# Kernel tuning notes

Hardware: AMD Instinct MI355X
Metric: run time of the kernel (lower is better)

## Reference

```python
import jax, jax.numpy as jnp
import numpy as np

N = 6144
IN_F = 128
OUT_F = 128
H = 4
OUT_PER_HEAD = OUT_F // H  # 32
ALPHA = 0.2  # leaky relu slope
NEG_BIG = -9e15


def setup_inputs() -> dict:
    key = jax.random.key(0)
    k1, k2, k3, k4 = jax.random.split(key, 4)
    h_mat = jax.random.normal(k1, (N, IN_F), dtype=jnp.float32)
    adj = (jax.random.uniform(k2, (N, N)) < 0.05).astype(jnp.float32)
    # glorot-ish scaled params
    weight = jax.random.normal(k3, (IN_F, H * OUT_PER_HEAD), dtype=jnp.float32) * (1.0 / np.sqrt(IN_F))
    att_weight = jax.random.normal(k4, (H, 2 * OUT_PER_HEAD), dtype=jnp.float32) * (1.0 / np.sqrt(OUT_PER_HEAD))
    return {"h_mat": h_mat, "adj": adj, "weight": weight, "att_weight": att_weight}


def reference(h_mat, adj, weight, att_weight):
    n = h_mat.shape[0]
    # W h : [n, H, f]
    wh = jnp.matmul(h_mat, weight).reshape(n, H, OUT_PER_HEAD)
    a_src = att_weight[:, :OUT_PER_HEAD]   # [H, f]
    a_dst = att_weight[:, OUT_PER_HEAD:]   # [H, f]
    logit_parent = jnp.einsum("nhf,hf->nh", wh, a_src)  # [n, H]
    logit_child = jnp.einsum("nhf,hf->nh", wh, a_dst)   # [n, H]
    # e_{ij,h} = leaky_relu(parent_i + child_j) : [n, n, H]
    e = jax.nn.leaky_relu(logit_parent[:, None, :] + logit_child[None, :, :], ALPHA)
    att = jnp.where(adj[..., None] > 0, e, NEG_BIG)
    att = jax.nn.softmax(att, axis=1)  # softmax over source nodes j
    # dropout is identity in inference mode (enable_dropout=False)
    h_prime = jnp.einsum("njh,jhf->nhf", att, wh)
    return h_prime.reshape(n, -1)  # concat=True -> [n, out_features]
```

## Files before the change

kernel.cpp:

```cpp
#include <hip/hip_runtime.h>
#include <hip/hip_bf16.h>
#include <stdint.h>
#include <stddef.h>

#define GN 6144
#define GH 4
#define HALF 3072
#define MAXD2 256

typedef float  f32x2  __attribute__((ext_vector_type(2)));
typedef float  f32x4  __attribute__((ext_vector_type(4)));
typedef float  f32x16 __attribute__((ext_vector_type(16)));
typedef __bf16 bf16x8 __attribute__((ext_vector_type(8)));

__device__ __forceinline__ float fast_exp2(float x) {
#if __has_builtin(__builtin_amdgcn_exp2f)
  return __builtin_amdgcn_exp2f(x);
#else
  return exp2f(x);
#endif
}

__global__ __launch_bounds__(256) void gat_wh(const float* __restrict__ hm,
                                              const float* __restrict__ wgt,
                                              const float* __restrict__ aw,
                                              __bf16* __restrict__ whR,
                                              float* __restrict__ lp2,
                                              float* __restrict__ lc2) {
  __shared__ float ldsC[64 * 132];
  const int t = threadIdx.x;
  const int wave = t >> 6, lane = t & 63;
  const int col = lane & 31, kg = lane >> 5;
  const int n0 = blockIdx.x * 64;
  const int rowHalf = (wave & 1) * 32;
  const int colBase = (wave >> 1) * 64;

  f32x16 acc[2];
#pragma unroll
  for (int ct = 0; ct < 2; ++ct)
#pragma unroll
    for (int i = 0; i < 16; ++i) acc[ct][i] = 0.0f;

#pragma unroll
  for (int kk = 0; kk < 8; ++kk) {
    const int k = kk * 16 + kg * 8;
    const f32x4 h0 = *(const f32x4*)(hm + (size_t)(n0 + rowHalf + col) * 128 + k);
    const f32x4 h1 = *(const f32x4*)(hm + (size_t)(n0 + rowHalf + col) * 128 + k + 4);
    bf16x8 af;
#pragma unroll
    for (int e = 0; e < 4; ++e) { af[e] = (__bf16)h0[e]; af[e + 4] = (__bf16)h1[e]; }
#pragma unroll
    for (int ct = 0; ct < 2; ++ct) {
      bf16x8 bfr;
#pragma unroll
      for (int e = 0; e < 8; ++e)
        bfr[e] = (__bf16)wgt[(size_t)(k + e) * 128 + colBase + ct * 32 + col];
      acc[ct] = __builtin_amdgcn_mfma_f32_32x32x16_bf16(af, bfr, acc[ct], 0, 0, 0);
    }
  }
#pragma unroll
  for (int ct = 0; ct < 2; ++ct)
#pragma unroll
    for (int r = 0; r < 16; ++r)
      ldsC[(rowHalf + (r & 3) + 8 * (r >> 2) + 4 * kg) * 132 + colBase + ct * 32 + col] =
          acc[ct][r];
  __syncthreads();

  {
    const int rr = t >> 2, cg = (t & 3) * 32;
    __bf16* dst = whR + (size_t)(n0 + rr) * 128 + cg;
#pragma unroll
    for (int q = 0; q < 4; ++q) {
      bf16x8 v;
#pragma unroll
      for (int e = 0; e < 8; ++e) v[e] = (__bf16)ldsC[rr * 132 + cg + q * 8 + e];
      *(bf16x8*)(dst + q * 8) = v;
    }
  }
  {
    const int nl = t & 63, h = t >> 6;
    float sp = 0.f, sd = 0.f;
#pragma unroll
    for (int f = 0; f < 32; ++f) {
      const float v = ldsC[nl * 132 + h * 32 + f];
      sp = fmaf(v, aw[h * 64 + f], sp);
      sd = fmaf(v, aw[h * 64 + 32 + f], sd);
    }
    const float LOG2E = 1.4426950408889634f;
    lp2[(n0 + nl) * GH + h] = sp * LOG2E;
    lc2[(n0 + nl) * GH + h] = sd * LOG2E;
  }
}

__global__ __launch_bounds__(256) void gat_fused(const float* __restrict__ adj,
                                                 const __bf16* __restrict__ whR,
                                                 const float* __restrict__ lp2,
                                                 const float* __restrict__ lc2,
                                                 float* __restrict__ out) {
  __shared__ unsigned short jidx[4][MAXD2];
  __shared__ float els[4][256];
  __shared__ float accx[4][64][2];
  __shared__ float denx[4][4];
  const int t = threadIdx.x, wave = t >> 6, lane = t & 63;
  const int row = blockIdx.x * 2 + (wave >> 1);
  const int half = wave & 1;
  const float* arow = adj + (size_t)row * GN + half * HALF;

  unsigned base = 0;
  f32x4 a0 = *(const f32x4*)(arow + lane * 4);
  f32x4 a1 = *(const f32x4*)(arow + 256 + lane * 4);
  for (int c = 0; c < 12; ++c) {
    f32x4 a2;
    if (c + 2 < 12) a2 = *(const f32x4*)(arow + (c + 2) * 256 + lane * 4);
#pragma unroll
    for (int s = 0; s < 4; ++s) {
      const bool p = a0[s] > 0.f;
      const unsigned long long m = __ballot(p);
      const unsigned rank = (unsigned)__popcll(m & ((1ull << lane) - 1ull));
      const unsigned pos = base + rank;
      if (p && pos < MAXD2)
        jidx[wave][pos] = (unsigned short)(half * HALF + c * 256 + lane * 4 + s);
      base += (unsigned)__popcll(m);
    }
    a0 = a1; a1 = a2;
  }
  int dg = (int)base;
  if (dg > MAXD2) dg = MAXD2;
  for (int k = dg + lane; k < MAXD2; k += 64) jidx[wave][k] = 0;

  const f32x4 lpv = *(const f32x4*)(lp2 + (size_t)row * GH);
  const int hsel = lane >> 4;
  float acc0 = 0.f, acc1 = 0.f;
  f32x2 d01 = f32x2{0.f, 0.f}, d23 = f32x2{0.f, 0.f};

  const int nch = (dg + 63) >> 6;
  for (int c = 0; c < nch; ++c) {
    const int k = c * 64 + lane;
    const bool valid = k < dg;
    const int jv = valid ? (int)jidx[wave][k] : 0;
    const f32x4 lc = *(const f32x4*)(lc2 + (size_t)jv * GH);

    f32x2 x01 = f32x2{lpv[0] + lc[0], lpv[1] + lc[1]};
    f32x2 x23 = f32x2{lpv[2] + lc[2], lpv[3] + lc[3]};
    x01 = __builtin_elementwise_max(x01, x01 * 0.2f);
    x23 = __builtin_elementwise_max(x23, x23 * 0.2f);
    const float vf = valid ? 1.f : 0.f;
    const f32x2 e01 = f32x2{fast_exp2(x01[0]), fast_exp2(x01[1])} * vf;
    const f32x2 e23 = f32x2{fast_exp2(x23[0]), fast_exp2(x23[1])} * vf;
    d01 += e01; d23 += e23;
    *(f32x4*)&els[wave][lane * 4] = f32x4{e01[0], e01[1], e23[0], e23[1]};

    const int lim = (dg - c * 64 < 64) ? (dg - c * 64) : 64;
    for (int k2 = 0; k2 < lim; k2 += 4) {
#pragma unroll
      for (int u = 0; u < 4; ++u) {
        const int jj = (int)jidx[wave][c * 64 + k2 + u];
        const unsigned wb = *(const unsigned*)(whR + (size_t)jj * 128 + lane * 2);
        const float eb = els[wave][(k2 + u) * 4 + hsel];
        const float wlo = __uint_as_float(wb << 16);
        const float whi = __uint_as_float(wb & 0xffff0000u);
        acc0 = fmaf(eb, wlo, acc0);
        acc1 = fmaf(eb, whi, acc1);
      }
    }
  }

  f32x4 dv = f32x4{d01[0], d01[1], d23[0], d23[1]};
#pragma unroll
  for (int off = 1; off < 64; off <<= 1) {
    dv[0] += __shfl_xor(dv[0], off);
    dv[1] += __shfl_xor(dv[1], off);
    dv[2] += __shfl_xor(dv[2], off);
    dv[3] += __shfl_xor(dv[3], off);
  }

  *(f32x2*)&accx[wave][lane][0] = f32x2{acc0, acc1};
  if (lane == 0) *(f32x4*)&denx[wave][0] = dv;
  __syncthreads();
  if ((wave & 1) == 0) {
    const float pa0 = accx[wave + 1][lane][0];
    const float pa1 = accx[wave + 1][lane][1];
    const float den = denx[wave][hsel] + denx[wave + 1][hsel];
    const float inv = 1.0f / den;
    const f32x2 o = f32x2{(acc0 + pa0) * inv, (acc1 + pa1) * inv};
    *(f32x2*)(out + (size_t)row * 128 + lane * 2) = o;
  }
}

extern "C" void kernel_launch(void* const* d_in, const int* in_sizes, int n_in,
                              void* d_out, int out_size, void* d_ws, size_t ws_size,
                              hipStream_t stream) {
  const float* hm  = (const float*)d_in[0];
  const float* adj = (const float*)d_in[1];
  const float* wgt = (const float*)d_in[2];
  const float* aw  = (const float*)d_in[3];
  float* out = (float*)d_out;

  char* ws = (char*)d_ws;
  __bf16* whR = (__bf16*)ws; ws += (size_t)GN * 128 * 2;
  float* lp2  = (float*)ws;  ws += GN * GH * 4;
  float* lc2  = (float*)ws;  ws += GN * GH * 4;

  gat_wh<<<96, 256, 0, stream>>>(hm, wgt, aw, whR, lp2, lc2);
  gat_fused<<<GN / 2, 256, 0, stream>>>(adj, whR, lp2, lc2, out);
}
```

Measured before the change: 62.96 us.

## Split gather across 4 lane groups with 16-byte row loads and shuffle reduction

Restructures the aggregation loop so each wave processes four neighbors at once. Each 16-lane group loads a full 256-byte bf16 row of Wh with 16-byte vector loads instead of 4-byte per-lane loads. It always iterates 16 groups per chunk, relying on zero-padded attention weights for invalid slots. The partial sums are then reduced across groups with xor shuffles. This cuts serial loop iterations and LDS index reads, but adds register pressure and reduction overhead, and does wasted work on partially filled chunks.

```diff
diff --git a/kernel.cpp b/kernel.cpp
--- a/kernel.cpp
+++ b/kernel.cpp
@@ -8,10 +8,11 @@
 #define HALF 3072
 #define MAXD2 256
 
-typedef float  f32x2  __attribute__((ext_vector_type(2)));
-typedef float  f32x4  __attribute__((ext_vector_type(4)));
-typedef float  f32x16 __attribute__((ext_vector_type(16)));
-typedef __bf16 bf16x8 __attribute__((ext_vector_type(8)));
+typedef float    f32x2  __attribute__((ext_vector_type(2)));
+typedef float    f32x4  __attribute__((ext_vector_type(4)));
+typedef float    f32x16 __attribute__((ext_vector_type(16)));
+typedef unsigned u32x4  __attribute__((ext_vector_type(4)));
+typedef __bf16   bf16x8 __attribute__((ext_vector_type(8)));
 
 __device__ __forceinline__ float fast_exp2(float x) {
 #if __has_builtin(__builtin_amdgcn_exp2f)
@@ -99,7 +100,7 @@
                                                  float* __restrict__ out) {
   __shared__ unsigned short jidx[4][MAXD2];
   __shared__ float els[4][256];
-  __shared__ float accx[4][64][2];
+  __shared__ float accx[4][16][8];
   __shared__ float denx[4][4];
   const int t = threadIdx.x, wave = t >> 6, lane = t & 63;
   const int row = blockIdx.x * 2 + (wave >> 1);
@@ -129,8 +130,11 @@
   for (int k = dg + lane; k < MAXD2; k += 64) jidx[wave][k] = 0;
 
   const f32x4 lpv = *(const f32x4*)(lp2 + (size_t)row * GH);
-  const int hsel = lane >> 4;
-  float acc0 = 0.f, acc1 = 0.f;
+  const int qlane = lane & 15;
+  const int elane = lane >> 4;
+  const int hsel = qlane >> 2;
+  f32x4 accA = f32x4{0.f, 0.f, 0.f, 0.f};
+  f32x4 accB = f32x4{0.f, 0.f, 0.f, 0.f};
   f32x2 d01 = f32x2{0.f, 0.f}, d23 = f32x2{0.f, 0.f};
 
   const int nch = (dg + 63) >> 6;
@@ -150,21 +154,35 @@
     d01 += e01; d23 += e23;
     *(f32x4*)&els[wave][lane * 4] = f32x4{e01[0], e01[1], e23[0], e23[1]};
 
-    const int lim = (dg - c * 64 < 64) ? (dg - c * 64) : 64;
-    for (int k2 = 0; k2 < lim; k2 += 4) {
-#pragma unroll
-      for (int u = 0; u < 4; ++u) {
-        const int jj = (int)jidx[wave][c * 64 + k2 + u];
-        const unsigned wb = *(const unsigned*)(whR + (size_t)jj * 128 + lane * 2);
-        const float eb = els[wave][(k2 + u) * 4 + hsel];
-        const float wlo = __uint_as_float(wb << 16);
-        const float whi = __uint_as_float(wb & 0xffff0000u);
-        acc0 = fmaf(eb, wlo, acc0);
-        acc1 = fmaf(eb, whi, acc1);
+#pragma unroll 4
+    for (int g = 0; g < 16; ++g) {
+      const int es = g * 4 + elane;
+      const int jj = (int)jidx[wave][c * 64 + es];
+      const u32x4 wb = *(const u32x4*)(whR + (size_t)jj * 128 + qlane * 8);
+      const float eb = els[wave][es * 4 + hsel];
+#pragma unroll
+      for (int w = 0; w < 4; ++w) {
+        const float wlo = __uint_as_float(wb[w] << 16);
+        const float whi = __uint_as_float(wb[w] & 0xffff0000u);
+        if (w < 2) {
+          accA[2 * w]     = fmaf(eb, wlo, accA[2 * w]);
+          accA[2 * w + 1] = fmaf(eb, whi, accA[2 * w + 1]);
+        } else {
+          accB[2 * w - 4] = fmaf(eb, wlo, accB[2 * w - 4]);
+          accB[2 * w - 3] = fmaf(eb, whi, accB[2 * w - 3]);
+        }
       }
     }
   }
 
+#pragma unroll
+  for (int off = 16; off <= 32; off <<= 1) {
+#pragma unroll
+    for (int e = 0; e < 4; ++e) {
+      accA[e] += __shfl_xor(accA[e], off);
+      accB[e] += __shfl_xor(accB[e], off);
+    }
+  }
   f32x4 dv = f32x4{d01[0], d01[1], d23[0], d23[1]};
 #pragma unroll
   for (int off = 1; off < 64; off <<= 1) {
@@ -174,16 +192,19 @@
     dv[3] += __shfl_xor(dv[3], off);
   }
 
-  *(f32x2*)&accx[wave][lane][0] = f32x2{acc0, acc1};
+  if (lane < 16) {
+    *(f32x4*)&accx[wave][qlane][0] = accA;
+    *(f32x4*)&accx[wave][qlane][4] = accB;
+  }
   if (lane == 0) *(f32x4*)&denx[wave][0] = dv;
   __syncthreads();
-  if ((wave & 1) == 0) {
-    const float pa0 = accx[wave + 1][lane][0];
-    const float pa1 = accx[wave + 1][lane][1];
+  if ((wave & 1) == 0 && lane < 16) {
+    const f32x4 pA = *(const f32x4*)&accx[wave + 1][qlane][0];
+    const f32x4 pB = *(const f32x4*)&accx[wave + 1][qlane][4];
     const float den = denx[wave][hsel] + denx[wave + 1][hsel];
     const float inv = 1.0f / den;
-    const f32x2 o = f32x2{(acc0 + pa0) * inv, (acc1 + pa1) * inv};
-    *(f32x2*)(out + (size_t)row * 128 + lane * 2) = o;
+    *(f32x4*)(out + (size_t)row * 128 + qlane * 8)     = (accA + pA) * inv;
+    *(f32x4*)(out + (size_t)row * 128 + qlane * 8 + 4) = (accB + pB) * inv;
   }
 }
 
```

Result: faster. 55.88 us (-11.2%).
